# Performance work log

Hardware: AMD Instinct MI355X
Metric: run time of the kernel (lower is better)

The kernel has to match this reference:

```python
import jax, jax.numpy as jnp
import numpy as np

N_HEAD = 12
M_HIST = 5      # Anderson history window (AndersonAcceleration.m)
BETA = 1.0      # Anderson mixing (AndersonAcceleration.beta)
LN_EPS = 1e-5


def _layer_norm(x, w, b):
    mu = x.mean(-1, keepdims=True)
    xc = x - mu
    var = (xc * xc).mean(-1, keepdims=True)
    return xc * jax.lax.rsqrt(var + LN_EPS) * w + b


def _mha(x, wqkv, bqkv, wo, bo):
    # torch nn.MultiheadAttention, batch_first, self-attention, no mask, dropout=0
    B, T, C = x.shape
    dh = C // N_HEAD
    qkv = x @ wqkv.T + bqkv                       # [B,T,3C]
    q, k, v = jnp.split(qkv, 3, axis=-1)
    def heads(t):
        return t.reshape(B, T, N_HEAD, dh).transpose(0, 2, 1, 3)  # [B,H,T,dh]
    q, k, v = heads(q), heads(k), heads(v)
    scores = jnp.einsum('bhqd,bhkd->bhqk', q, k) / jnp.sqrt(jnp.asarray(dh, x.dtype))
    att = jax.nn.softmax(scores, axis=-1)
    out = jnp.einsum('bhqk,bhkd->bhqd', att, v).transpose(0, 2, 1, 3).reshape(B, T, C)
    return out @ wo.T + bo


def _deq_delta(z, u, emb_row, ln1_w, ln1_b, in_proj_w, in_proj_b, out_proj_w,
               out_proj_b, ln2_w, ln2_b, mlp_w1, mlp_b1, mlp_w2, mlp_b2):
    # DEQOperator.forward -> delta_z
    z_temporal = z + 0.1 * emb_row                 # broadcast [C] over [B,T,C]
    z_ctx = z_temporal + u
    x = _layer_norm(z_ctx, ln1_w, ln1_b)
    attn_out = _mha(x, in_proj_w, in_proj_b, out_proj_w, out_proj_b)
    z_attn = z + attn_out
    h = _layer_norm(z_attn, ln2_w, ln2_b)
    h = jax.nn.gelu(h @ mlp_w1.T + mlp_b1, approximate=False) @ mlp_w2.T + mlp_b2
    z_mlp = z_attn + h
    return z_mlp - z


def _deq_solve(u, iter_emb, ln1_w, ln1_b, in_proj_w, in_proj_b, out_proj_w,
               out_proj_b, ln2_w, ln2_b, mlp_w1, mlp_b1, mlp_w2, mlp_b2, num_iters):
    B, T, C = u.shape
    z = jnp.zeros_like(u)
    Xs, Fs = [], []   # Anderson history of states / residuals
    max_row = iter_emb.shape[0] - 1
    for it in range(num_iters):
        emb_row = iter_emb[min(it, max_row)]
        delta = _deq_delta(z, u, emb_row, ln1_w, ln1_b, in_proj_w, in_proj_b,
                           out_proj_w, out_proj_b, ln2_w, ln2_b,
                           mlp_w1, mlp_b1, mlp_w2, mlp_b2)
        res = delta  # residual of f(z) = z + delta_z w.r.t. z
        Xs.append(z); Fs.append(res)
        if len(Xs) > M_HIST:
            Xs.pop(0); Fs.pop(0)
        if len(Xs) == 1:
            z = z + BETA * res
        else:
            K = len(Xs) - 1
            dF = jnp.stack(Fs[:-1], 0) - res[None]               # [K,B,T,C]
            dF_f = dF.transpose(1, 2, 0, 3).reshape(B * T, K, C)  # per-token LS
            r_f = res.reshape(B * T, C)
            G = jnp.einsum('nkc,nlc->nkl', dF_f, dF_f)            # [BT,K,K]
            G = G + 1e-6 * jnp.eye(K, dtype=u.dtype)
            bvec = jnp.einsum('nkc,nc->nk', dF_f, r_f)            # [BT,K]
            alpha = jnp.linalg.solve(G, bvec[..., None])[..., 0]
            d = r_f - jnp.einsum('nkc,nk->nc', dF_f, alpha)
            z = (z.reshape(B * T, C) + BETA * d).reshape(B, T, C)
    return z


def setup_inputs() -> dict:
    key = jax.random.key(0)
    ks = jax.random.split(key, 6)
    B, T, C = 4, 1024, 768
    std = 0.02
    return {
        'u': jax.random.normal(ks[0], (B, T, C), jnp.float32),
        'iter_emb': std * jax.random.normal(ks[1], (31, C), jnp.float32),
        'ln1_w': jnp.ones((C,), jnp.float32),
        'ln1_b': jnp.zeros((C,), jnp.float32),
        'in_proj_w': std * jax.random.normal(ks[2], (3 * C, C), jnp.float32),
        'in_proj_b': jnp.zeros((3 * C,), jnp.float32),
        'out_proj_w': std * jax.random.normal(ks[3], (C, C), jnp.float32),
        'out_proj_b': jnp.zeros((C,), jnp.float32),
        'ln2_w': jnp.ones((C,), jnp.float32),
        'ln2_b': jnp.zeros((C,), jnp.float32),
        'mlp_w1': std * jax.random.normal(ks[4], (4 * C, C), jnp.float32),
        'mlp_b1': jnp.zeros((4 * C,), jnp.float32),
        'mlp_w2': std * jax.random.normal(ks[5], (C, 4 * C), jnp.float32),
        'mlp_b2': jnp.zeros((C,), jnp.float32),
        'num_iters': 6,
    }


def reference(u, iter_emb, ln1_w, ln1_b, in_proj_w, in_proj_b, out_proj_w,
              out_proj_b, ln2_w, ln2_b, mlp_w1, mlp_b1, mlp_w2, mlp_b2, num_iters):
    return _deq_solve(u, iter_emb, ln1_w, ln1_b, in_proj_w, in_proj_b,
                      out_proj_w, out_proj_b, ln2_w, ln2_b,
                      mlp_w1, mlp_b1, mlp_w2, mlp_b2, int(num_iters))
```

## Files before the change

kernel.cpp:

```cpp
#include <hip/hip_runtime.h>
#include <math.h>

#define BT 4096
#define CDIM 768
#define NHEAD 12
#define DH 64
#define TSEQ 1024
#define BBATCH 4

typedef _Float16 f16;
typedef __attribute__((ext_vector_type(4))) _Float16 f16x4;
typedef __attribute__((ext_vector_type(8))) _Float16 f16x8;
typedef __attribute__((ext_vector_type(4))) float f32x4;

__device__ __forceinline__ float block_reduce_sum(float v, float* sbuf) {
#pragma unroll
  for (int o = 32; o > 0; o >>= 1) v += __shfl_down(v, o, 64);
  int lane = threadIdx.x & 63;
  int w = threadIdx.x >> 6;
  if (lane == 0) sbuf[w] = v;
  __syncthreads();
  float r = sbuf[0] + sbuf[1] + sbuf[2] + sbuf[3];
  __syncthreads();
  return r;
}

__global__ __launch_bounds__(256) void zero_kernel(float4* __restrict__ p) {
  p[(size_t)blockIdx.x * 256 + threadIdx.x] = make_float4(0.f, 0.f, 0.f, 0.f);
}

__global__ __launch_bounds__(256) void cvt_f16_kernel(
    const float* __restrict__ in, f16* __restrict__ out) {
  size_t i = ((size_t)blockIdx.x * 256 + threadIdx.x) * 4;
  float4 v = *(const float4*)(in + i);
  f16x4 o = {(f16)v.x, (f16)v.y, (f16)v.z, (f16)v.w};
  *(f16x4*)(out + i) = o;
}

__global__ __launch_bounds__(256) void ln1_kernel(
    const float* __restrict__ z, const float* __restrict__ u,
    const float* __restrict__ emb, const float* __restrict__ w,
    const float* __restrict__ b, f16* __restrict__ x) {
  __shared__ float sbuf[4];
  int row = blockIdx.x;
  int tid = threadIdx.x;
  const float* zr = z + (size_t)row * CDIM;
  const float* ur = u + (size_t)row * CDIM;
  float v[3];
  float s = 0.f;
#pragma unroll
  for (int i = 0; i < 3; i++) {
    int c = tid + i * 256;
    v[i] = zr[c] + 0.1f * emb[c] + ur[c];
    s += v[i];
  }
  s = block_reduce_sum(s, sbuf);
  float mu = s * (1.f / CDIM);
  float sq = 0.f;
#pragma unroll
  for (int i = 0; i < 3; i++) { v[i] -= mu; sq += v[i] * v[i]; }
  sq = block_reduce_sum(sq, sbuf);
  float rstd = rsqrtf(sq * (1.f / CDIM) + 1e-5f);
  f16* xr = x + (size_t)row * CDIM;
#pragma unroll
  for (int i = 0; i < 3; i++) {
    int c = tid + i * 256;
    xr[c] = (f16)(v[i] * rstd * w[c] + b[c]);
  }
}

__global__ __launch_bounds__(256) void ln2_kernel(
    const float* __restrict__ in, const float* __restrict__ w,
    const float* __restrict__ b, f16* __restrict__ x) {
  __shared__ float sbuf[4];
  int row = blockIdx.x;
  int tid = threadIdx.x;
  const float* ir = in + (size_t)row * CDIM;
  float v[3];
  float s = 0.f;
#pragma unroll
  for (int i = 0; i < 3; i++) {
    int c = tid + i * 256;
    v[i] = ir[c];
    s += v[i];
  }
  s = block_reduce_sum(s, sbuf);
  float mu = s * (1.f / CDIM);
  float sq = 0.f;
#pragma unroll
  for (int i = 0; i < 3; i++) { v[i] -= mu; sq += v[i] * v[i]; }
  sq = block_reduce_sum(sq, sbuf);
  float rstd = rsqrtf(sq * (1.f / CDIM) + 1e-5f);
  f16* xr = x + (size_t)row * CDIM;
#pragma unroll
  for (int i = 0; i < 3; i++) {
    int c = tid + i * 256;
    xr[c] = (f16)(v[i] * rstd * w[c] + b[c]);
  }
}

__device__ __forceinline__ float gelu_exact(float t) {
  return 0.5f * t * (1.f + erff(t * 0.70710678118654752f));
}

#define GS128 72
template <int MODE>
__global__ __launch_bounds__(256, 3) void gemm_mfma(
    const f16* __restrict__ A, const f16* __restrict__ W,
    const float* __restrict__ bias, f16* __restrict__ hq,
    f16* __restrict__ hk, f16* __restrict__ hvt, f16* __restrict__ hout,
    int M, int N, int K) {
  __shared__ __align__(16) f16 As[128 * GS128];
  __shared__ __align__(16) f16 Bs[128 * GS128];
  int tid = threadIdx.x;
  int wv = tid >> 6, lane = tid & 63;
  int bm = blockIdx.y, bn = blockIdx.x;
  int wm = (wv >> 1) * 64, wn = (wv & 1) * 64;

  int srow = tid >> 3;
  int scol = (tid & 7) * 8;
  const f16* gA = A + (size_t)(bm * 128 + srow) * K + scol;
  const f16* gB = W + (size_t)(bn * 128 + srow) * K + scol;

  f32x4 acc[4][4];
#pragma unroll
  for (int i = 0; i < 4; i++)
#pragma unroll
    for (int j = 0; j < 4; j++) acc[i][j] = (f32x4){0.f, 0.f, 0.f, 0.f};

  int am = lane & 15;
  int quad = lane >> 4;
  int ak = quad * 8;

  f16x8 ar[4], br[4];
#pragma unroll
  for (int c = 0; c < 4; c++) {
    ar[c] = *(const f16x8*)(gA + (size_t)(c * 32) * K);
    br[c] = *(const f16x8*)(gB + (size_t)(c * 32) * K);
  }

  for (int k0 = 0; k0 < K; k0 += 64) {
    __syncthreads();
#pragma unroll
    for (int c = 0; c < 4; c++) {
      *(f16x8*)&As[(srow + c * 32) * GS128 + scol] = ar[c];
      *(f16x8*)&Bs[(srow + c * 32) * GS128 + scol] = br[c];
    }
    __syncthreads();
    int kn = k0 + 64;
    if (kn < K) {
#pragma unroll
      for (int c = 0; c < 4; c++) {
        ar[c] = *(const f16x8*)(gA + (size_t)(c * 32) * K + kn);
        br[c] = *(const f16x8*)(gB + (size_t)(c * 32) * K + kn);
      }
    }
#pragma unroll
    for (int kk = 0; kk < 2; kk++) {
      f16x8 af[4], bfr[4];
#pragma unroll
      for (int mi = 0; mi < 4; mi++)
        af[mi] = *(const f16x8*)&As[(wm + mi * 16 + am) * GS128 + kk * 32 + ak];
#pragma unroll
      for (int nj = 0; nj < 4; nj++)
        bfr[nj] = *(const f16x8*)&Bs[(wn + nj * 16 + am) * GS128 + kk * 32 + ak];
#pragma unroll
      for (int mi = 0; mi < 4; mi++)
#pragma unroll
        for (int nj = 0; nj < 4; nj++)
          acc[mi][nj] = __builtin_amdgcn_mfma_f32_16x16x32_f16(
              af[mi], bfr[nj], acc[mi][nj], 0, 0, 0);
    }
  }

  int crow0 = bm * 128 + wm + quad * 4;
  int ccol0 = bn * 128 + wn + am;
#pragma unroll
  for (int nj = 0; nj < 4; nj++) {
    int col = ccol0 + nj * 16;
    float bcol = bias[col];
    if constexpr (MODE == 3) {
      int which = col / CDIM;
      int rem = col - which * CDIM;
      int h = rem >> 6;
      int d = rem & 63;
#pragma unroll
      for (int mi = 0; mi < 4; mi++) {
#pragma unroll
        for (int r = 0; r < 4; r++) {
          int m = crow0 + mi * 16 + r;
          int bb = m >> 10, t = m & 1023;
          f16 val = (f16)(acc[mi][nj][r] + bcol);
          if (which == 0)
            hq[(((size_t)(bb * NHEAD + h) * TSEQ + t) << 6) + d] = val;
          else if (which == 1)
            hk[(((size_t)(bb * NHEAD + h) * TSEQ + t) << 6) + d] = val;
          else
            hvt[(((size_t)(bb * NHEAD + h) * DH + d) << 10) + t] = val;
        }
      }
    } else {
#pragma unroll
      for (int mi = 0; mi < 4; mi++) {
#pragma unroll
        for (int r = 0; r < 4; r++) {
          int m = crow0 + mi * 16 + r;
          size_t idx = (size_t)m * N + col;
          hout[idx] = (f16)gelu_exact(acc[mi][nj][r] + bcol);
        }
      }
    }
  }
}

#define GS 72
template <int MODE>
__global__ __launch_bounds__(256, 4) void gemm_mfma64(
    const f16* __restrict__ A, const f16* __restrict__ W,
    const float* __restrict__ bias, const float* __restrict__ aux1,
    const float* __restrict__ aux2, float* __restrict__ fout0,
    int M, int N, int K) {
  __shared__ __align__(16) f16 As[64 * GS];
  __shared__ __align__(16) f16 Bs[64 * GS];
  int tid = threadIdx.x;
  int wv = tid >> 6, lane = tid & 63;
  int bm = blockIdx.x, bn = blockIdx.y;
  int wm = (wv >> 1) * 32, wn = (wv & 1) * 32;

  int srow = tid >> 2;
  int scol = (tid & 3) * 16;
  const f16* gA = A + (size_t)(bm * 64 + srow) * K + scol;
  const f16* gB = W + (size_t)(bn * 64 + srow) * K + scol;

  f32x4 acc[2][2];
#pragma unroll
  for (int i = 0; i < 2; i++)
#pragma unroll
    for (int j = 0; j < 2; j++) acc[i][j] = (f32x4){0.f, 0.f, 0.f, 0.f};

  int am = lane & 15;
  int ak = (lane >> 4) * 8;

  f16x8 a0 = *(const f16x8*)(gA);
  f16x8 a1 = *(const f16x8*)(gA + 8);
  f16x8 b0 = *(const f16x8*)(gB);
  f16x8 b1 = *(const f16x8*)(gB + 8);

  for (int k0 = 0; k0 < K; k0 += 64) {
    __syncthreads();
    *(f16x8*)&As[srow * GS + scol] = a0;
    *(f16x8*)&As[srow * GS + scol + 8] = a1;
    *(f16x8*)&Bs[srow * GS + scol] = b0;
    *(f16x8*)&Bs[srow * GS + scol + 8] = b1;
    __syncthreads();
    int kn = k0 + 64;
    if (kn < K) {
      a0 = *(const f16x8*)(gA + kn);
      a1 = *(const f16x8*)(gA + kn + 8);
      b0 = *(const f16x8*)(gB + kn);
      b1 = *(const f16x8*)(gB + kn + 8);
    }
#pragma unroll
    for (int kk = 0; kk < 2; kk++) {
      f16x8 af[2], bfr[2];
#pragma unroll
      for (int mi = 0; mi < 2; mi++)
        af[mi] = *(const f16x8*)&As[(wm + mi * 16 + am) * GS + kk * 32 + ak];
#pragma unroll
      for (int nj = 0; nj < 2; nj++)
        bfr[nj] = *(const f16x8*)&Bs[(wn + nj * 16 + am) * GS + kk * 32 + ak];
#pragma unroll
      for (int mi = 0; mi < 2; mi++)
#pragma unroll
        for (int nj = 0; nj < 2; nj++)
          acc[mi][nj] = __builtin_amdgcn_mfma_f32_16x16x32_f16(
              af[mi], bfr[nj], acc[mi][nj], 0, 0, 0);
    }
  }

  int crow0 = bm * 64 + wm + (lane >> 4) * 4;
  int ccol0 = bn * 64 + wn + (lane & 15);
#pragma unroll
  for (int nj = 0; nj < 2; nj++) {
    int col = ccol0 + nj * 16;
    float bcol = bias[col];
#pragma unroll
    for (int mi = 0; mi < 2; mi++) {
#pragma unroll
      for (int r = 0; r < 4; r++) {
        int m = crow0 + mi * 16 + r;
        size_t idx = (size_t)m * N + col;
        float val = acc[mi][nj][r] + bcol;
        if constexpr (MODE == 0) {
          fout0[idx] = val + aux1[idx];
        } else {
          fout0[idx] = val + aux1[idx] - aux2[idx];
        }
      }
    }
  }
}

#define PSTRIDE 72
#define KVS 72
__global__ __launch_bounds__(256, 3) void flash_attn8(
    const f16* __restrict__ Qg, const f16* __restrict__ Kg,
    const f16* __restrict__ Vt, f16* __restrict__ attn) {
  __shared__ __align__(16) f16 Ks[64 * KVS];
  __shared__ __align__(16) f16 Vs[64 * KVS];
  __shared__ __align__(16) f16 Plds[4][16 * PSTRIDE];
  int tid = threadIdx.x;
  int wv = tid >> 6, lane = tid & 63;
  int bh = blockIdx.x;
  int bb = bh / NHEAD, h = bh % NHEAD;
  int m0 = (blockIdx.y * 4 + wv) * 16;
  int am = lane & 15;
  int quad = lane >> 4;
  int ak = quad * 8;

  int srow = tid >> 3;
  int scol = (tid & 7) * 8;

  const f16* kb = Kg + (((size_t)bh * TSEQ) << 6);
  const f16* vb = Vt + (((size_t)bh * DH) << 10);

  const f16* qbase = Qg + (((size_t)bh * TSEQ + m0) << 6);
  f16x8 qf0 = *(const f16x8*)(qbase + am * 64 + ak);
  f16x8 qf1 = *(const f16x8*)(qbase + am * 64 + 32 + ak);
#pragma unroll
  for (int i = 0; i < 8; i++) { qf0[i] *= (f16)0.125f; qf1[i] *= (f16)0.125f; }

  f16* Pw = Plds[wv];
  f32x4 Oa[4];
#pragma unroll
  for (int i = 0; i < 4; i++) Oa[i] = (f32x4){0.f, 0.f, 0.f, 0.f};
  float lpart[4] = {0.f, 0.f, 0.f, 0.f};

  f16x8 kr0 = *(const f16x8*)(kb + (size_t)srow * 64 + scol);
  f16x8 kr1 = *(const f16x8*)(kb + (size_t)(32 + srow) * 64 + scol);
  f16x8 vr0 = *(const f16x8*)(vb + (size_t)srow * TSEQ + scol);
  f16x8 vr1 = *(const f16x8*)(vb + (size_t)(32 + srow) * TSEQ + scol);

  for (int n0 = 0; n0 < TSEQ; n0 += 64) {
    __syncthreads();
    *(f16x8*)&Ks[srow * KVS + scol] = kr0;
    *(f16x8*)&Ks[(32 + srow) * KVS + scol] = kr1;
    *(f16x8*)&Vs[srow * KVS + scol] = vr0;
    *(f16x8*)&Vs[(32 + srow) * KVS + scol] = vr1;
    __syncthreads();
    int nn = n0 + 64;
    if (nn < TSEQ) {
      kr0 = *(const f16x8*)(kb + (size_t)(nn + srow) * 64 + scol);
      kr1 = *(const f16x8*)(kb + (size_t)(nn + 32 + srow) * 64 + scol);
      vr0 = *(const f16x8*)(vb + (size_t)srow * TSEQ + nn + scol);
      vr1 = *(const f16x8*)(vb + (size_t)(32 + srow) * TSEQ + nn + scol);
    }
    f32x4 S[4];
#pragma unroll
    for (int t = 0; t < 4; t++) {
      f16x8 kf0 = *(const f16x8*)&Ks[(16 * t + am) * KVS + ak];
      f16x8 kf1 = *(const f16x8*)&Ks[(16 * t + am) * KVS + 32 + ak];
      S[t] = __builtin_amdgcn_mfma_f32_16x16x32_f16(
          qf0, kf0, (f32x4){0.f, 0.f, 0.f, 0.f}, 0, 0, 0);
      S[t] = __builtin_amdgcn_mfma_f32_16x16x32_f16(qf1, kf1, S[t], 0, 0, 0);
    }
#pragma unroll
    for (int t = 0; t < 4; t++) {
#pragma unroll
      for (int r = 0; r < 4; r++) {
        float p = __expf(S[t][r]);
        lpart[r] += p;
        Pw[(quad * 4 + r) * PSTRIDE + 16 * t + am] = (f16)p;
      }
    }
    f16x8 pa0 = *(const f16x8*)&Pw[am * PSTRIDE + ak];
    f16x8 pa1 = *(const f16x8*)&Pw[am * PSTRIDE + 32 + ak];
#pragma unroll
    for (int dt = 0; dt < 4; dt++) {
      f16x8 vf0 = *(const f16x8*)&Vs[(16 * dt + am) * KVS + ak];
      f16x8 vf1 = *(const f16x8*)&Vs[(16 * dt + am) * KVS + 32 + ak];
      Oa[dt] = __builtin_amdgcn_mfma_f32_16x16x32_f16(pa0, vf0, Oa[dt], 0, 0, 0);
      Oa[dt] = __builtin_amdgcn_mfma_f32_16x16x32_f16(pa1, vf1, Oa[dt], 0, 0, 0);
    }
  }

#pragma unroll
  for (int o = 1; o < 16; o <<= 1)
#pragma unroll
    for (int r = 0; r < 4; r++) lpart[r] += __shfl_xor(lpart[r], o, 64);

#pragma unroll
  for (int r = 0; r < 4; r++) {
    int m = m0 + quad * 4 + r;
    float inv = 1.f / lpart[r];
    f16* orow = attn + ((size_t)(bb * TSEQ + m)) * CDIM + h * DH;
#pragma unroll
    for (int dt = 0; dt < 4; dt++)
      orow[dt * 16 + am] = (f16)(Oa[dt][r] * inv);
  }
}

__global__ __launch_bounds__(256) void add_res_kernel(
    float* __restrict__ z, const float* __restrict__ r) {
  size_t i = (size_t)blockIdx.x * 256 + threadIdx.x;
  z[i] += r[i];
}

template <int KA>
__global__ __launch_bounds__(256) void anderson_kernel(
    float* __restrict__ z, const float* __restrict__ rescur,
    const float* __restrict__ p0, const float* __restrict__ p1,
    const float* __restrict__ p2, const float* __restrict__ p3) {
  __shared__ float sbuf[4];
  int row = blockIdx.x, tid = threadIdx.x;
  size_t base = (size_t)row * CDIM + tid;
  float r[3];
#pragma unroll
  for (int i = 0; i < 3; i++) r[i] = rescur[base + i * 256];
  const float* ps[4] = {p0, p1, p2, p3};
  float dF[KA][3];
#pragma unroll
  for (int k = 0; k < KA; k++)
#pragma unroll
    for (int i = 0; i < 3; i++) dF[k][i] = ps[k][base + i * 256] - r[i];

  float Gm[KA][KA], bv[KA];
#pragma unroll
  for (int k = 0; k < KA; k++) {
#pragma unroll
    for (int ll = k; ll < KA; ll++) {
      float p = 0.f;
#pragma unroll
      for (int i = 0; i < 3; i++) p += dF[k][i] * dF[ll][i];
      float t = block_reduce_sum(p, sbuf);
      Gm[k][ll] = t;
      Gm[ll][k] = t;
    }
  }
#pragma unroll
  for (int k = 0; k < KA; k++) Gm[k][k] += 1e-6f;
#pragma unroll
  for (int k = 0; k < KA; k++) {
    float p = 0.f;
#pragma unroll
    for (int i = 0; i < 3; i++) p += dF[k][i] * r[i];
    bv[k] = block_reduce_sum(p, sbuf);
  }
  float alpha[KA];
#pragma unroll
  for (int p = 0; p < KA; p++) {
    float inv = 1.f / Gm[p][p];
#pragma unroll
    for (int rr = p + 1; rr < KA; rr++) {
      float f = Gm[rr][p] * inv;
#pragma unroll
      for (int c = p; c < KA; c++) Gm[rr][c] -= f * Gm[p][c];
      bv[rr] -= f * bv[p];
    }
  }
#pragma unroll
  for (int p = KA - 1; p >= 0; p--) {
    float s2 = bv[p];
#pragma unroll
    for (int c = p + 1; c < KA; c++) s2 -= Gm[p][c] * alpha[c];
    alpha[p] = s2 / Gm[p][p];
  }
#pragma unroll
  for (int i = 0; i < 3; i++) {
    float d = r[i];
#pragma unroll
    for (int k = 0; k < KA; k++) d = fmaf(-dF[k][i], alpha[k], d);
    z[base + i * 256] += d;
  }
}

extern "C" void kernel_launch(void* const* d_in, const int* in_sizes, int n_in,
                              void* d_out, int out_size, void* d_ws,
                              size_t ws_size, hipStream_t stream) {
  (void)in_sizes; (void)n_in; (void)out_size; (void)ws_size;
  const float* u = (const float*)d_in[0];
  const float* iter_emb = (const float*)d_in[1];
  const float* ln1w = (const float*)d_in[2];
  const float* ln1b = (const float*)d_in[3];
  const float* wqkv = (const float*)d_in[4];
  const float* bqkv = (const float*)d_in[5];
  const float* wo = (const float*)d_in[6];
  const float* bo = (const float*)d_in[7];
  const float* ln2w = (const float*)d_in[8];
  const float* ln2b = (const float*)d_in[9];
  const float* w1 = (const float*)d_in[10];
  const float* b1 = (const float*)d_in[11];
  const float* w2 = (const float*)d_in[12];
  const float* b2 = (const float*)d_in[13];

  const size_t S = (size_t)BT * CDIM;
  float* ws = (float*)d_ws;
  float* z = ws + 0 * S;
  float* zattn = ws + 1 * S;
  float* res[5] = {ws + 2 * S, ws + 3 * S, ws + 4 * S, ws + 5 * S, ws + 6 * S};
  f16* q_h = (f16*)(ws + 7 * S);
  f16* k_h = q_h + S;
  f16* vt_h = q_h + 2 * S;
  f16* h_h = (f16*)(ws + 7 * S);
  f16* x_h = (f16*)(ws + 9 * S);
  f16* wqkv_h = x_h + S;
  f16* wo_h = wqkv_h + (size_t)3 * CDIM * CDIM;
  f16* w1_h = wo_h + (size_t)CDIM * CDIM;
  f16* w2_h = w1_h + (size_t)4 * CDIM * CDIM;

  cvt_f16_kernel<<<1728, 256, 0, stream>>>(wqkv, wqkv_h);
  cvt_f16_kernel<<<576, 256, 0, stream>>>(wo, wo_h);
  cvt_f16_kernel<<<2304, 256, 0, stream>>>(w1, w1_h);
  cvt_f16_kernel<<<2304, 256, 0, stream>>>(w2, w2_h);
  zero_kernel<<<S / 1024, 256, 0, stream>>>((float4*)z);

  for (int it = 0; it < 6; it++) {
    ln1_kernel<<<BT, 256, 0, stream>>>(z, u, iter_emb + it * CDIM, ln1w, ln1b,
                                       x_h);
    gemm_mfma<3><<<dim3(18, 32), 256, 0, stream>>>(
        x_h, wqkv_h, bqkv, q_h, k_h, vt_h, nullptr, BT, 3 * CDIM, CDIM);
    flash_attn8<<<dim3(BBATCH * NHEAD, TSEQ / 64), 256, 0, stream>>>(
        q_h, k_h, vt_h, x_h);
    gemm_mfma64<0><<<dim3(64, 12), 256, 0, stream>>>(
        x_h, wo_h, bo, z, nullptr, zattn, BT, CDIM, CDIM);
    ln2_kernel<<<BT, 256, 0, stream>>>(zattn, ln2w, ln2b, x_h);
    gemm_mfma<1><<<dim3(24, 32), 256, 0, stream>>>(
        x_h, w1_h, b1, nullptr, nullptr, nullptr, h_h, BT, 4 * CDIM, CDIM);
    float* rcur = res[it % 5];
    gemm_mfma64<2><<<dim3(64, 12), 256, 0, stream>>>(
        h_h, w2_h, b2, zattn, z, rcur, BT, CDIM, 4 * CDIM);

    int Kh = it < 4 ? it : 4;
    if (Kh == 0) {
      add_res_kernel<<<S / 256, 256, 0, stream>>>(z, rcur);
    } else {
      const float* p[4] = {rcur, rcur, rcur, rcur};
      for (int kx = 1; kx <= Kh; kx++) p[kx - 1] = res[(it - kx) % 5];
      switch (Kh) {
        case 1: anderson_kernel<1><<<BT, 256, 0, stream>>>(z, rcur, p[0], p[1], p[2], p[3]); break;
        case 2: anderson_kernel<2><<<BT, 256, 0, stream>>>(z, rcur, p[0], p[1], p[2], p[3]); break;
        case 3: anderson_kernel<3><<<BT, 256, 0, stream>>>(z, rcur, p[0], p[1], p[2], p[3]); break;
        default: anderson_kernel<4><<<BT, 256, 0, stream>>>(z, rcur, p[0], p[1], p[2], p[3]); break;
      }
    }
  }
  hipMemcpyAsync(d_out, z, S * sizeof(float), hipMemcpyDeviceToDevice, stream);
}
```

Measured before the change: 1.224 ms.

## Split-K the MLP down-projection with atomics, prefill residual in LN2

Replaces the 64x64-tile down-projection GEMM (K=3072) with a 128x128-tile split-K kernel that splits K into 4 chunks and accumulates partial results with atomic float adds. The residual base (zattn - z + b2) is written by the LN2 kernel, which now has to run first so the atomics add onto an initialised buffer. This aims to raise per-block arithmetic intensity and still keep enough blocks (768) to fill the device. The cost is atomic traffic to global memory, non-deterministic summation order, and an extra residual write in LN2.

Result: slower. 1.271 ms (+3.8%).

```diff
diff --git a/kernel.cpp b/kernel.cpp
--- a/kernel.cpp
+++ b/kernel.cpp
@@ -71,17 +71,22 @@
 
 __global__ __launch_bounds__(256) void ln2_kernel(
     const float* __restrict__ in, const float* __restrict__ w,
-    const float* __restrict__ b, f16* __restrict__ x) {
+    const float* __restrict__ b, f16* __restrict__ x,
+    const float* __restrict__ z, const float* __restrict__ b2,
+    float* __restrict__ rinit) {
   __shared__ float sbuf[4];
   int row = blockIdx.x;
   int tid = threadIdx.x;
   const float* ir = in + (size_t)row * CDIM;
+  const float* zr = z + (size_t)row * CDIM;
+  float* rr = rinit + (size_t)row * CDIM;
   float v[3];
   float s = 0.f;
 #pragma unroll
   for (int i = 0; i < 3; i++) {
     int c = tid + i * 256;
     v[i] = ir[c];
+    rr[c] = v[i] - zr[c] + b2[c];
     s += v[i];
   }
   s = block_reduce_sum(s, sbuf);
@@ -208,6 +213,95 @@
           size_t idx = (size_t)m * N + col;
           hout[idx] = (f16)gelu_exact(acc[mi][nj][r] + bcol);
         }
+      }
+    }
+  }
+}
+
+#define KSPLIT 4
+#define KCHUNK 768
+__global__ __launch_bounds__(256, 3) void gemm_splitk(
+    const f16* __restrict__ A, const f16* __restrict__ W,
+    float* __restrict__ out, int N, int Ktot) {
+  __shared__ __align__(16) f16 As[128 * GS128];
+  __shared__ __align__(16) f16 Bs[128 * GS128];
+  int b = blockIdx.x;
+  int n = (b & 7) * 96 + (b >> 3);
+  int bn = n % 6;
+  int bm = (n / 6) & 31;
+  int ks = n / 192;
+
+  int tid = threadIdx.x;
+  int wv = tid >> 6, lane = tid & 63;
+  int wm = (wv >> 1) * 64, wn = (wv & 1) * 64;
+
+  int srow = tid >> 3;
+  int scol = (tid & 7) * 8;
+  const f16* gA = A + (size_t)(bm * 128 + srow) * Ktot + ks * KCHUNK + scol;
+  const f16* gB = W + (size_t)(bn * 128 + srow) * Ktot + ks * KCHUNK + scol;
+
+  f32x4 acc[4][4];
+#pragma unroll
+  for (int i = 0; i < 4; i++)
+#pragma unroll
+    for (int j = 0; j < 4; j++) acc[i][j] = (f32x4){0.f, 0.f, 0.f, 0.f};
+
+  int am = lane & 15;
+  int quad = lane >> 4;
+  int ak = quad * 8;
+
+  f16x8 ar[4], br[4];
+#pragma unroll
+  for (int c = 0; c < 4; c++) {
+    ar[c] = *(const f16x8*)(gA + (size_t)(c * 32) * Ktot);
+    br[c] = *(const f16x8*)(gB + (size_t)(c * 32) * Ktot);
+  }
+
+  for (int k0 = 0; k0 < KCHUNK; k0 += 64) {
+    __syncthreads();
+#pragma unroll
+    for (int c = 0; c < 4; c++) {
+      *(f16x8*)&As[(srow + c * 32) * GS128 + scol] = ar[c];
+      *(f16x8*)&Bs[(srow + c * 32) * GS128 + scol] = br[c];
+    }
+    __syncthreads();
+    int kn = k0 + 64;
+    if (kn < KCHUNK) {
+#pragma unroll
+      for (int c = 0; c < 4; c++) {
+        ar[c] = *(const f16x8*)(gA + (size_t)(c * 32) * Ktot + kn);
+        br[c] = *(const f16x8*)(gB + (size_t)(c * 32) * Ktot + kn);
+      }
+    }
+#pragma unroll
+    for (int kk = 0; kk < 2; kk++) {
+      f16x8 af[4], bfr[4];
+#pragma unroll
+      for (int mi = 0; mi < 4; mi++)
+        af[mi] = *(const f16x8*)&As[(wm + mi * 16 + am) * GS128 + kk * 32 + ak];
+#pragma unroll
+      for (int nj = 0; nj < 4; nj++)
+        bfr[nj] = *(const f16x8*)&Bs[(wn + nj * 16 + am) * GS128 + kk * 32 + ak];
+#pragma unroll
+      for (int mi = 0; mi < 4; mi++)
+#pragma unroll
+        for (int nj = 0; nj < 4; nj++)
+          acc[mi][nj] = __builtin_amdgcn_mfma_f32_16x16x32_f16(
+              af[mi], bfr[nj], acc[mi][nj], 0, 0, 0);
+    }
+  }
+
+  int crow0 = bm * 128 + wm + quad * 4;
+  int ccol0 = wn + am;
+#pragma unroll
+  for (int nj = 0; nj < 4; nj++) {
+    int col = bn * 128 + ccol0 + nj * 16;
+#pragma unroll
+    for (int mi = 0; mi < 4; mi++) {
+#pragma unroll
+      for (int r = 0; r < 4; r++) {
+        int m = crow0 + mi * 16 + r;
+        unsafeAtomicAdd(out + (size_t)m * N + col, acc[mi][nj][r]);
       }
     }
   }
@@ -515,6 +609,7 @@
   zero_kernel<<<S / 1024, 256, 0, stream>>>((float4*)z);
 
   for (int it = 0; it < 6; it++) {
+    float* rcur = res[it % 5];
     ln1_kernel<<<BT, 256, 0, stream>>>(z, u, iter_emb + it * CDIM, ln1w, ln1b,
                                        x_h);
     gemm_mfma<3><<<dim3(18, 32), 256, 0, stream>>>(
@@ -523,12 +618,11 @@
         q_h, k_h, vt_h, x_h);
     gemm_mfma64<0><<<dim3(64, 12), 256, 0, stream>>>(
         x_h, wo_h, bo, z, nullptr, zattn, BT, CDIM, CDIM);
-    ln2_kernel<<<BT, 256, 0, stream>>>(zattn, ln2w, ln2b, x_h);
+    ln2_kernel<<<BT, 256, 0, stream>>>(zattn, ln2w, ln2b, x_h, z, b2, rcur);
     gemm_mfma<1><<<dim3(24, 32), 256, 0, stream>>>(
         x_h, w1_h, b1, nullptr, nullptr, nullptr, h_h, BT, 4 * CDIM, CDIM);
-    float* rcur = res[it % 5];
-    gemm_mfma64<2><<<dim3(64, 12), 256, 0, stream>>>(
-        h_h, w2_h, b2, zattn, z, rcur, BT, CDIM, 4 * CDIM);
+    gemm_splitk<<<dim3(6 * 32 * KSPLIT), 256, 0, stream>>>(
+        h_h, w2_h, rcur, CDIM, 4 * CDIM);
 
     int Kh = it < 4 ? it : 4;
     if (Kh == 0) {
```

## Fuse Anderson update with next LN1, split-K MLP2 with atomics, raise occupancy

Applied to the files above, without the earlier changes.

Fuses the Anderson mixing step with the following iteration's LayerNorm-1, so z is not re-read by a separate kernel. The residual is pre-initialised in LN2 (zattn - z + b2), and the second MLP GEMM becomes a two-way split-K kernel that atomically adds its partial products into the residual. Launch bounds are raised for the 128-tile GEMM and the split-K GEMM to allow more resident blocks. The changes remove kernel launches and memory passes and give the tall-K GEMM more parallelism. In exchange they add atomic traffic, make the floating-point sum order nondeterministic, and may cause register spills under the tighter launch bounds.

Result: slower. 1.516 ms (+23.8%).

```diff
diff --git a/kernel.cpp b/kernel.cpp
--- a/kernel.cpp
+++ b/kernel.cpp
@@ -71,17 +71,22 @@
 
 __global__ __launch_bounds__(256) void ln2_kernel(
     const float* __restrict__ in, const float* __restrict__ w,
-    const float* __restrict__ b, f16* __restrict__ x) {
+    const float* __restrict__ b, f16* __restrict__ x,
+    const float* __restrict__ z, const float* __restrict__ b2,
+    float* __restrict__ rinit) {
   __shared__ float sbuf[4];
   int row = blockIdx.x;
   int tid = threadIdx.x;
   const float* ir = in + (size_t)row * CDIM;
+  const float* zr = z + (size_t)row * CDIM;
+  float* rr = rinit + (size_t)row * CDIM;
   float v[3];
   float s = 0.f;
 #pragma unroll
   for (int i = 0; i < 3; i++) {
     int c = tid + i * 256;
     v[i] = ir[c];
+    rr[c] = v[i] - zr[c] + b2[c];
     s += v[i];
   }
   s = block_reduce_sum(s, sbuf);
@@ -105,7 +110,7 @@
 
 #define GS128 72
 template <int MODE>
-__global__ __launch_bounds__(256, 3) void gemm_mfma(
+__global__ __launch_bounds__(256, 4) void gemm_mfma(
     const f16* __restrict__ A, const f16* __restrict__ W,
     const float* __restrict__ bias, f16* __restrict__ hq,
     f16* __restrict__ hk, f16* __restrict__ hvt, f16* __restrict__ hout,
@@ -215,11 +220,10 @@
 
 #define GS 72
 template <int MODE>
-__global__ __launch_bounds__(256, 4) void gemm_mfma64(
+__global__ __launch_bounds__(256, (MODE == 4) ? 6 : 4) void gemm_mfma64(
     const f16* __restrict__ A, const f16* __restrict__ W,
     const float* __restrict__ bias, const float* __restrict__ aux1,
-    const float* __restrict__ aux2, float* __restrict__ fout0,
-    int M, int N, int K) {
+    float* __restrict__ fout0, int M, int N, int K) {
   __shared__ __align__(16) f16 As[64 * GS];
   __shared__ __align__(16) f16 Bs[64 * GS];
   int tid = threadIdx.x;
@@ -227,10 +231,13 @@
   int bm = blockIdx.x, bn = blockIdx.y;
   int wm = (wv >> 1) * 32, wn = (wv & 1) * 32;
 
+  int ks = (MODE == 4) ? blockIdx.z : 0;
+  int kl = (MODE == 4) ? (K >> 1) : K;
+
   int srow = tid >> 2;
   int scol = (tid & 3) * 16;
-  const f16* gA = A + (size_t)(bm * 64 + srow) * K + scol;
-  const f16* gB = W + (size_t)(bn * 64 + srow) * K + scol;
+  const f16* gA = A + (size_t)(bm * 64 + srow) * K + ks * kl + scol;
+  const f16* gB = W + (size_t)(bn * 64 + srow) * K + ks * kl + scol;
 
   f32x4 acc[2][2];
 #pragma unroll
@@ -246,7 +253,7 @@
   f16x8 b0 = *(const f16x8*)(gB);
   f16x8 b1 = *(const f16x8*)(gB + 8);
 
-  for (int k0 = 0; k0 < K; k0 += 64) {
+  for (int k0 = 0; k0 < kl; k0 += 64) {
     __syncthreads();
     *(f16x8*)&As[srow * GS + scol] = a0;
     *(f16x8*)&As[srow * GS + scol + 8] = a1;
@@ -254,7 +261,7 @@
     *(f16x8*)&Bs[srow * GS + scol + 8] = b1;
     __syncthreads();
     int kn = k0 + 64;
-    if (kn < K) {
+    if (kn < kl) {
       a0 = *(const f16x8*)(gA + kn);
       a1 = *(const f16x8*)(gA + kn + 8);
       b0 = *(const f16x8*)(gB + kn);
@@ -283,18 +290,17 @@
 #pragma unroll
   for (int nj = 0; nj < 2; nj++) {
     int col = ccol0 + nj * 16;
-    float bcol = bias[col];
+    float bcol = (MODE == 4) ? 0.f : bias[col];
 #pragma unroll
     for (int mi = 0; mi < 2; mi++) {
 #pragma unroll
       for (int r = 0; r < 4; r++) {
         int m = crow0 + mi * 16 + r;
         size_t idx = (size_t)m * N + col;
-        float val = acc[mi][nj][r] + bcol;
         if constexpr (MODE == 0) {
-          fout0[idx] = val + aux1[idx];
+          fout0[idx] = acc[mi][nj][r] + bcol + aux1[idx];
         } else {
-          fout0[idx] = val + aux1[idx] - aux2[idx];
+          unsafeAtomicAdd(fout0 + idx, acc[mi][nj][r]);
         }
       }
     }
@@ -400,10 +406,107 @@
   }
 }
 
-__global__ __launch_bounds__(256) void add_res_kernel(
-    float* __restrict__ z, const float* __restrict__ r) {
-  size_t i = (size_t)blockIdx.x * 256 + threadIdx.x;
-  z[i] += r[i];
+template <int KA>
+__global__ __launch_bounds__(256) void anderson_ln1(
+    float* __restrict__ z, const float* __restrict__ rescur,
+    const float* __restrict__ p0, const float* __restrict__ p1,
+    const float* __restrict__ p2, const float* __restrict__ p3,
+    const float* __restrict__ u, const float* __restrict__ emb,
+    const float* __restrict__ w, const float* __restrict__ b,
+    f16* __restrict__ x) {
+  __shared__ float sbuf[4];
+  int row = blockIdx.x, tid = threadIdx.x;
+  size_t base = (size_t)row * CDIM + tid;
+  float r[3];
+#pragma unroll
+  for (int i = 0; i < 3; i++) r[i] = rescur[base + i * 256];
+
+  float zn[3];
+  if constexpr (KA == 0) {
+#pragma unroll
+    for (int i = 0; i < 3; i++) zn[i] = z[base + i * 256] + r[i];
+  } else {
+    const float* ps[4] = {p0, p1, p2, p3};
+    float dF[KA == 0 ? 1 : KA][3];
+#pragma unroll
+    for (int k = 0; k < KA; k++)
+#pragma unroll
+      for (int i = 0; i < 3; i++) dF[k][i] = ps[k][base + i * 256] - r[i];
+
+    float Gm[KA == 0 ? 1 : KA][KA == 0 ? 1 : KA], bv[KA == 0 ? 1 : KA];
+#pragma unroll
+    for (int k = 0; k < KA; k++) {
+#pragma unroll
+      for (int ll = k; ll < KA; ll++) {
+        float p = 0.f;
+#pragma unroll
+        for (int i = 0; i < 3; i++) p += dF[k][i] * dF[ll][i];
+        float t = block_reduce_sum(p, sbuf);
+        Gm[k][ll] = t;
+        Gm[ll][k] = t;
+      }
+    }
+#pragma unroll
+    for (int k = 0; k < KA; k++) Gm[k][k] += 1e-6f;
+#pragma unroll
+    for (int k = 0; k < KA; k++) {
+      float p = 0.f;
+#pragma unroll
+      for (int i = 0; i < 3; i++) p += dF[k][i] * r[i];
+      bv[k] = block_reduce_sum(p, sbuf);
+    }
+    float alpha[KA == 0 ? 1 : KA];
+#pragma unroll
+    for (int p = 0; p < KA; p++) {
+      float inv = 1.f / Gm[p][p];
+#pragma unroll
+      for (int rr = p + 1; rr < KA; rr++) {
+        float f = Gm[rr][p] * inv;
+#pragma unroll
+        for (int c = p; c < KA; c++) Gm[rr][c] -= f * Gm[p][c];
+        bv[rr] -= f * bv[p];
+      }
+    }
+#pragma unroll
+    for (int p = KA - 1; p >= 0; p--) {
+      float s2 = bv[p];
+#pragma unroll
+      for (int c = p + 1; c < KA; c++) s2 -= Gm[p][c] * alpha[c];
+      alpha[p] = s2 / Gm[p][p];
+    }
+#pragma unroll
+    for (int i = 0; i < 3; i++) {
+      float d = r[i];
+#pragma unroll
+      for (int k = 0; k < KA; k++) d = fmaf(-dF[k][i], alpha[k], d);
+      zn[i] = z[base + i * 256] + d;
+    }
+  }
+#pragma unroll
+  for (int i = 0; i < 3; i++) z[base + i * 256] = zn[i];
+
+  const float* ur = u + (size_t)row * CDIM;
+  float v[3];
+  float s = 0.f;
+#pragma unroll
+  for (int i = 0; i < 3; i++) {
+    int c = tid + i * 256;
+    v[i] = zn[i] + 0.1f * emb[c] + ur[c];
+    s += v[i];
+  }
+  s = block_reduce_sum(s, sbuf);
+  float mu = s * (1.f / CDIM);
+  float sq = 0.f;
+#pragma unroll
+  for (int i = 0; i < 3; i++) { v[i] -= mu; sq += v[i] * v[i]; }
+  sq = block_reduce_sum(sq, sbuf);
+  float rstd = rsqrtf(sq * (1.f / CDIM) + 1e-5f);
+  f16* xr = x + (size_t)row * CDIM;
+#pragma unroll
+  for (int i = 0; i < 3; i++) {
+    int c = tid + i * 256;
+    xr[c] = (f16)(v[i] * rstd * w[c] + b[c]);
+  }
 }
 
 template <int KA>
@@ -515,33 +618,36 @@
   zero_kernel<<<S / 1024, 256, 0, stream>>>((float4*)z);
 
   for (int it = 0; it < 6; it++) {
-    ln1_kernel<<<BT, 256, 0, stream>>>(z, u, iter_emb + it * CDIM, ln1w, ln1b,
-                                       x_h);
+    float* rcur = res[it % 5];
+    if (it == 0) {
+      ln1_kernel<<<BT, 256, 0, stream>>>(z, u, iter_emb, ln1w, ln1b, x_h);
+    }
     gemm_mfma<3><<<dim3(18, 32), 256, 0, stream>>>(
         x_h, wqkv_h, bqkv, q_h, k_h, vt_h, nullptr, BT, 3 * CDIM, CDIM);
     flash_attn8<<<dim3(BBATCH * NHEAD, TSEQ / 64), 256, 0, stream>>>(
         q_h, k_h, vt_h, x_h);
     gemm_mfma64<0><<<dim3(64, 12), 256, 0, stream>>>(
-        x_h, wo_h, bo, z, nullptr, zattn, BT, CDIM, CDIM);
-    ln2_kernel<<<BT, 256, 0, stream>>>(zattn, ln2w, ln2b, x_h);
+        x_h, wo_h, bo, z, zattn, BT, CDIM, CDIM);
+    ln2_kernel<<<BT, 256, 0, stream>>>(zattn, ln2w, ln2b, x_h, z, b2, rcur);
     gemm_mfma<1><<<dim3(24, 32), 256, 0, stream>>>(
         x_h, w1_h, b1, nullptr, nullptr, nullptr, h_h, BT, 4 * CDIM, CDIM);
-    float* rcur = res[it % 5];
-    gemm_mfma64<2><<<dim3(64, 12), 256, 0, stream>>>(
-        h_h, w2_h, b2, zattn, z, rcur, BT, CDIM, 4 * CDIM);
+    gemm_mfma64<4><<<dim3(64, 12, 2), 256, 0, stream>>>(
+        h_h, w2_h, b2, nullptr, rcur, BT, CDIM, 4 * CDIM);
 
     int Kh = it < 4 ? it : 4;
-    if (Kh == 0) {
-      add_res_kernel<<<S / 256, 256, 0, stream>>>(z, rcur);
+    const float* p[4] = {rcur, rcur, rcur, rcur};
+    for (int kx = 1; kx <= Kh; kx++) p[kx - 1] = res[(it - kx) % 5];
+    if (it < 5) {
+      const float* embn = iter_emb + (it + 1) * CDIM;
+      switch (Kh) {
+        case 0: anderson_ln1<0><<<BT, 256, 0, stream>>>(z, rcur, p[0], p[1], p[2], p[3], u, embn, ln1w, ln1b, x_h); break;
+        case 1: anderson_ln1<1><<<BT, 256, 0, stream>>>(z, rcur, p[0], p[1], p[2], p[3], u, embn, ln1w, ln1b, x_h); break;
+        case 2: anderson_ln1<2><<<BT, 256, 0, stream>>>(z, rcur, p[0], p[1], p[2], p[3], u, embn, ln1w, ln1b, x_h); break;
+        case 3: anderson_ln1<3><<<BT, 256, 0, stream>>>(z, rcur, p[0], p[1], p[2], p[3], u, embn, ln1w, ln1b, x_h); break;
+        default: anderson_ln1<4><<<BT, 256, 0, stream>>>(z, rcur, p[0], p[1], p[2], p[3], u, embn, ln1w, ln1b, x_h); break;
+      }
     } else {
-      const float* p[4] = {rcur, rcur, rcur, rcur};
-      for (int kx = 1; kx <= Kh; kx++) p[kx - 1] = res[(it - kx) % 5];
-      switch (Kh) {
-        case 1: anderson_kernel<1><<<BT, 256, 0, stream>>>(z, rcur, p[0], p[1], p[2], p[3]); break;
-        case 2: anderson_kernel<2><<<BT, 256, 0, stream>>>(z, rcur, p[0], p[1], p[2], p[3]); break;
-        case 3: anderson_kernel<3><<<BT, 256, 0, stream>>>(z, rcur, p[0], p[1], p[2], p[3]); break;
-        default: anderson_kernel<4><<<BT, 256, 0, stream>>>(z, rcur, p[0], p[1], p[2], p[3]); break;
-      }
+      anderson_kernel<4><<<BT, 256, 0, stream>>>(z, rcur, p[0], p[1], p[2], p[3]);
     }
   }
   hipMemcpyAsync(d_out, z, S * sizeof(float), hipMemcpyDeviceToDevice, stream);
```
